# Kernel optimization log

Hardware: AMD Instinct MI355X
Metric: run time of the kernel (lower is better)

The kernel has to match this reference:

```python
import jax, jax.numpy as jnp
import numpy as np

NSTEPS = 20
ALPHA, BETA = 0.9, 0.85


def setup_inputs() -> dict:
    key = jax.random.key(0)
    ks = jax.random.split(key, 12)
    B, T, D_in, K, OUT = 64, NSTEPS, 16384, 25, 2
    dims = [8192, 4096, 2048]      # floor(dim/factor) per layer, factor=2
    prev = [16384, 8192, 4096]     # fan-in width each layer gathers from
    std = (2.0 / K) ** 0.5
    inp = {"x": jax.random.normal(ks[0], (B, T, D_in), jnp.float32)}
    for i, (d, p) in enumerate(zip(dims, prev)):
        inp[f"W{i}"] = jax.random.normal(ks[1 + i], (d, K), jnp.float32) * std
        inp[f"b{i}"] = jnp.zeros((1, d), jnp.float32)
        inp[f"knn{i}"] = jax.random.randint(ks[4 + i], (d, K), 0, p)
        inp[f"thr{i}"] = jax.random.uniform(ks[7 + i], (d,), jnp.float32)
    inp["Wfc"] = jax.random.normal(ks[10], (OUT, dims[-1]), jnp.float32) * dims[-1] ** -0.5
    inp["bfc"] = jnp.zeros((OUT,), jnp.float32)
    return inp


def reference(x, W0, b0, W1, b1, W2, b2, knn0, knn1, knn2,
              thr0, thr1, thr2, Wfc, bfc):
    # x: (B, T, D_in) -> scan over T
    Ws, bs = (W0, W1, W2), (b0, b1, b2)
    knns, thrs = (knn0, knn1, knn2), (thr0, thr1, thr2)
    n_layer = 3
    B = x.shape[0]
    xs = jnp.transpose(x, (1, 0, 2))  # (T, B, D_in)
    mems0 = tuple(jnp.zeros((B, w.shape[0]), x.dtype) for w in Ws)

    def step(mems, xt):
        h = xt
        new_mems, mem_recs, spk_recs = [], [], []
        for i in range(n_layer):
            g = h[:, knns[i]]                             # (B, dim_i, K) gather
            cur = jnp.einsum('bdk,dk->bd', g, Ws[i]) + bs[i]
            thr, mem_prev = thrs[i], mems[i]
            reset = (mem_prev > thr).astype(h.dtype)
            # NOTE: original code never writes the returned syn back, so the
            # synaptic state stays at zero init: syn = alpha*0 + cur = cur.
            syn = cur
            mem = BETA * mem_prev + syn - reset * thr
            spk = (mem - thr > 0).astype(h.dtype)
            if i == n_layer - 1:
                h = mem                 # last layer passes membrane forward
                new_mems.append(mem_prev)  # last-layer carry never updated
            else:
                h = spk
                new_mems.append(mem)
            mem_recs.append(mem)
            spk_recs.append(spk)
        angle = h @ Wfc.T + bfc
        return tuple(new_mems), (tuple(mem_recs), tuple(spk_recs), angle)

    _, (mem_rec, spk_rec, angles_all) = jax.lax.scan(step, mems0, xs)
    angles = angles_all[-1]  # original keeps only the last step's angle
    return (*mem_rec, *spk_rec, angles)
```

## Files before the change

kernel.cpp:

```cpp
#include <hip/hip_runtime.h>

#define NSTEPS 20
#define BATCH 64
#define D_IN 16384
#define KNN 25
#define BETA 0.85

#define D0 8192
#define D1 4096
#define D2 2048

#define NRT 24

__global__ void __launch_bounds__(256) transpose_x_kernel(
    const float* __restrict__ x, float* __restrict__ xT) {
  __shared__ float tile[64][65];
  const int t = blockIdx.y;
  const int d0 = blockIdx.x * 64;
  {
    const int dd4 = (threadIdx.x & 15) * 4;
    const int br = threadIdx.x >> 4;
#pragma unroll
    for (int i = 0; i < 4; ++i) {
      const int b = br + 16 * i;
      const float4 v = *reinterpret_cast<const float4*>(
          &x[((size_t)b * NSTEPS + t) * D_IN + d0 + dd4]);
      tile[b][dd4 + 0] = v.x;
      tile[b][dd4 + 1] = v.y;
      tile[b][dd4 + 2] = v.z;
      tile[b][dd4 + 3] = v.w;
    }
  }
  __syncthreads();
  {
    const int b = threadIdx.x & 63;
    const int dg = threadIdx.x >> 6;
#pragma unroll
    for (int i = 0; i < 16; ++i) {
      const int d = dg * 16 + i;
      xT[((size_t)t * D_IN + d0 + d) * BATCH + b] = tile[b][d];
    }
  }
}

template <bool IS_U8>
__global__ void __launch_bounds__(512) cur_kernel(
    const void* __restrict__ src, size_t st_t, const float* __restrict__ W,
    const float* __restrict__ bias, const int* __restrict__ knn, int dn,
    int dchunk0, double* __restrict__ curbuf) {
  const int nb_d = dn >> 4;
  const int g = blockIdx.x & 7;
  const int q = blockIdx.x >> 3;
  const int r = q / nb_d;
  const int i = q - r * nb_d;
  const int t = r * 8 + g;
  if (t >= NSTEPS) return;

  const int lane = threadIdx.x & 63;
  const int wv = threadIdx.x >> 6;
  const int dl0 = i * 16 + wv * 2;

#pragma unroll
  for (int j = 0; j < 2; ++j) {
    const int dl = dl0 + j;
    const int dg = __builtin_amdgcn_readfirstlane(dchunk0 + dl);
    const int* kp = knn + (size_t)dg * KNN;
    const float* wp = W + (size_t)dg * KNN;
    double cur = (double)bias[dg];
    if (IS_U8) {
      const unsigned char* sp =
          (const unsigned char*)src + (size_t)t * st_t + lane;
#pragma unroll
      for (int k = 0; k < KNN; ++k) {
        const int idx = kp[k];
        cur += (double)wp[k] * (double)sp[(size_t)idx * BATCH];
      }
    } else {
      const float* sp = (const float*)src + (size_t)t * st_t + lane;
#pragma unroll
      for (int k = 0; k < KNN; ++k) {
        const int idx = kp[k];
        cur += (double)wp[k] * (double)sp[(size_t)idx * BATCH];
      }
    }
    curbuf[((size_t)t * dn + dl) * BATCH + lane] = cur;
  }
}

__global__ void __launch_bounds__(512) scan_kernel(
    const double* __restrict__ curbuf, int dn, int dchunk0, int D,
    const float* __restrict__ thr, float* __restrict__ mem_rec,
    float* __restrict__ spk_rec, unsigned char* __restrict__ spkT) {
  __shared__ float s_mem[16][68];
  __shared__ float s_spk[16][68];
  const int dl0 = blockIdx.x * 16;
  const int lane = threadIdx.x & 63;
  const int wv = threadIdx.x >> 6;
  const int dbase = dl0 + wv * 2;

  double mem[2] = {0.0, 0.0};
  double thrv[2];
#pragma unroll
  for (int j = 0; j < 2; ++j) thrv[j] = (double)thr[dchunk0 + dbase + j];

  for (int t = 0; t < NSTEPS; ++t) {
#pragma unroll
    for (int j = 0; j < 2; ++j) {
      const int dl = dbase + j;
      const double cur = curbuf[((size_t)t * dn + dl) * BATCH + lane];
      double m = mem[j];
      const double reset = (m > thrv[j]) ? thrv[j] : 0.0;
      m = BETA * m + cur - reset;
      mem[j] = m;
      const float spk = (m > thrv[j]) ? 1.0f : 0.0f;
      s_mem[wv * 2 + j][lane] = (float)m;
      s_spk[wv * 2 + j][lane] = spk;
      if (spkT)
        spkT[((size_t)t * D + dchunk0 + dl) * BATCH + lane] =
            (unsigned char)spk;
    }
    __syncthreads();
    {
      const int dd = threadIdx.x & 15;
      const int bq = threadIdx.x >> 4;
#pragma unroll
      for (int i = 0; i < 2; ++i) {
        const int b = bq + 32 * i;
        const size_t o = ((size_t)t * BATCH + b) * D + dchunk0 + dl0 + dd;
        mem_rec[o] = s_mem[dd][b];
        spk_rec[o] = s_spk[dd][b];
      }
    }
    __syncthreads();
  }
}

template <bool IS_U8, bool CARRY>
__global__ void __launch_bounds__(512) layer_scan_kernel(
    const void* __restrict__ src, size_t st_t, size_t st_b, size_t st_idx,
    const float* __restrict__ W, const float* __restrict__ bias,
    const int* __restrict__ knn, const float* __restrict__ thr, int D,
    float* __restrict__ mem_rec, float* __restrict__ spk_rec,
    unsigned char* __restrict__ spkT) {
  __shared__ float s_mem[16][68];
  __shared__ float s_spk[16][68];
  const int d0 = blockIdx.x * 16;
  const int lane = threadIdx.x & 63;
  const int wv = threadIdx.x >> 6;
  const int dbase = d0 + wv * 2;

  double mem[2] = {0.0, 0.0};
  double thrv[2], bsv[2];
#pragma unroll
  for (int j = 0; j < 2; ++j) {
    thrv[j] = (double)thr[dbase + j];
    bsv[j] = (double)bias[dbase + j];
  }

  const int t_lo = CARRY ? 0 : (int)blockIdx.y;
  const int t_hi = CARRY ? NSTEPS : (int)blockIdx.y + 1;

  for (int t = t_lo; t < t_hi; ++t) {
#pragma unroll
    for (int j = 0; j < 2; ++j) {
      const int d = dbase + j;
      const int* kp = knn + (size_t)d * KNN;
      const float* wp = W + (size_t)d * KNN;
      const size_t base = (size_t)t * st_t + (size_t)lane * st_b;
      double cur = bsv[j];
#pragma unroll
      for (int k = 0; k < KNN; ++k) {
        const int idx = kp[k];
        if (IS_U8) {
          const unsigned char s =
              ((const unsigned char*)src)[base + (size_t)idx * st_idx];
          cur += (double)wp[k] * (double)s;
        } else {
          const float g = ((const float*)src)[base + (size_t)idx * st_idx];
          cur += (double)wp[k] * (double)g;
        }
      }
      double m = CARRY ? mem[j] : 0.0;
      const double reset = (m > thrv[j]) ? thrv[j] : 0.0;
      m = BETA * m + cur - reset;
      mem[j] = m;
      const float spk = (m > thrv[j]) ? 1.0f : 0.0f;
      s_mem[wv * 2 + j][lane] = (float)m;
      s_spk[wv * 2 + j][lane] = spk;
      if (spkT) spkT[((size_t)t * D + d) * BATCH + lane] = (unsigned char)spk;
    }
    __syncthreads();
    {
      const int dd = threadIdx.x & 15;
      const int bq = threadIdx.x >> 4;
#pragma unroll
      for (int i = 0; i < 2; ++i) {
        const int b = bq + 32 * i;
        const size_t o = ((size_t)t * BATCH + b) * D + d0 + dd;
        mem_rec[o] = s_mem[dd][b];
        spk_rec[o] = s_spk[dd][b];
      }
    }
    __syncthreads();
  }
}

__global__ void __launch_bounds__(64) fc_kernel(
    const float* __restrict__ mem2, const float* __restrict__ Wfc,
    const float* __restrict__ bfc, float* __restrict__ angles) {
  const int b = blockIdx.x;
  const float* h = mem2 + ((size_t)(NSTEPS - 1) * BATCH + b) * D2;
  double a0 = 0.0, a1 = 0.0;
  for (int d = threadIdx.x; d < D2; d += 64) {
    const double m = (double)h[d];
    a0 += m * (double)Wfc[d];
    a1 += m * (double)Wfc[D2 + d];
  }
#pragma unroll
  for (int off = 32; off > 0; off >>= 1) {
    a0 += __shfl_down(a0, off);
    a1 += __shfl_down(a1, off);
  }
  if (threadIdx.x == 0) {
    angles[(size_t)b * 2 + 0] = (float)(a0 + (double)bfc[0]);
    angles[(size_t)b * 2 + 1] = (float)(a1 + (double)bfc[1]);
  }
}

extern "C" void kernel_launch(void* const* d_in, const int* in_sizes, int n_in,
                              void* d_out, int out_size, void* d_ws,
                              size_t ws_size, hipStream_t stream) {
  const float* x = (const float*)d_in[0];
  const float* W0 = (const float*)d_in[1];
  const float* b0 = (const float*)d_in[2];
  const int* knn0 = (const int*)d_in[3];
  const float* thr0 = (const float*)d_in[4];
  const float* W1 = (const float*)d_in[5];
  const float* b1 = (const float*)d_in[6];
  const int* knn1 = (const int*)d_in[7];
  const float* thr1 = (const float*)d_in[8];
  const float* W2 = (const float*)d_in[9];
  const float* b2 = (const float*)d_in[10];
  const int* knn2 = (const int*)d_in[11];
  const float* thr2 = (const float*)d_in[12];
  const float* Wfc = (const float*)d_in[13];
  const float* bfc = (const float*)d_in[14];

  float* out = (float*)d_out;
  float* mem_rec0 = out;
  float* mem_rec1 = mem_rec0 + (size_t)NSTEPS * BATCH * D0;
  float* mem_rec2 = mem_rec1 + (size_t)NSTEPS * BATCH * D1;
  float* spk_rec0 = mem_rec2 + (size_t)NSTEPS * BATCH * D2;
  float* spk_rec1 = spk_rec0 + (size_t)NSTEPS * BATCH * D0;
  float* spk_rec2 = spk_rec1 + (size_t)NSTEPS * BATCH * D1;
  float* angles = spk_rec2 + (size_t)NSTEPS * BATCH * D2;

  const size_t xT_bytes = (size_t)NSTEPS * D_IN * BATCH * sizeof(float);
  const size_t s0_bytes = (size_t)NSTEPS * D0 * BATCH;
  const size_t s1_bytes = (size_t)NSTEPS * D1 * BATCH;
  const size_t base_bytes = xT_bytes + s0_bytes + s1_bytes;

  const bool planA = ws_size >= base_bytes;
  const bool planB = !planA && ws_size >= s0_bytes + s1_bytes;

  size_t leftover = (ws_size > base_bytes) ? ws_size - base_bytes : 0;
  int Dc = (int)((leftover / ((size_t)NSTEPS * BATCH * 8)) & ~(size_t)15);
  if (Dc > D0) Dc = D0;
  const bool planT = planA && Dc >= 512;

  const dim3 blk(512);

  if (planT) {
    float* xT = (float*)d_ws;
    unsigned char* spk0T = (unsigned char*)d_ws + xT_bytes;
    unsigned char* spk1T = spk0T + s0_bytes;
    double* curbuf = (double*)((char*)d_ws + base_bytes);

    transpose_x_kernel<<<dim3(D_IN / 64, NSTEPS), 256, 0, stream>>>(x, xT);

    for (int c0 = 0; c0 < D0; c0 += Dc) {
      const int dn = (D0 - c0 < Dc) ? (D0 - c0) : Dc;
      cur_kernel<false><<<dim3(NRT * (dn / 16)), blk, 0, stream>>>(
          xT, (size_t)D_IN * BATCH, W0, b0, knn0, dn, c0, curbuf);
      scan_kernel<<<dim3(dn / 16), blk, 0, stream>>>(
          curbuf, dn, c0, D0, thr0, mem_rec0, spk_rec0, spk0T);
    }
    for (int c0 = 0; c0 < D1; c0 += Dc) {
      const int dn = (D1 - c0 < Dc) ? (D1 - c0) : Dc;
      cur_kernel<true><<<dim3(NRT * (dn / 16)), blk, 0, stream>>>(
          spk0T, (size_t)D0 * BATCH, W1, b1, knn1, dn, c0, curbuf);
      scan_kernel<<<dim3(dn / 16), blk, 0, stream>>>(
          curbuf, dn, c0, D1, thr1, mem_rec1, spk_rec1, spk1T);
    }
    layer_scan_kernel<true, false><<<dim3(D2 / 16, NSTEPS), blk, 0, stream>>>(
        spk1T, (size_t)D1 * BATCH, 1, BATCH, W2, b2, knn2, thr2, D2, mem_rec2,
        spk_rec2, nullptr);
  } else if (planA) {
    float* xT = (float*)d_ws;
    unsigned char* spk0T = (unsigned char*)d_ws + xT_bytes;
    unsigned char* spk1T = spk0T + s0_bytes;

    transpose_x_kernel<<<dim3(D_IN / 64, NSTEPS), 256, 0, stream>>>(x, xT);
    layer_scan_kernel<false, true><<<dim3(D0 / 16), blk, 0, stream>>>(
        xT, (size_t)D_IN * BATCH, 1, BATCH, W0, b0, knn0, thr0, D0, mem_rec0,
        spk_rec0, spk0T);
    layer_scan_kernel<true, true><<<dim3(D1 / 16), blk, 0, stream>>>(
        spk0T, (size_t)D0 * BATCH, 1, BATCH, W1, b1, knn1, thr1, D1, mem_rec1,
        spk_rec1, spk1T);
    layer_scan_kernel<true, false><<<dim3(D2 / 16, NSTEPS), blk, 0, stream>>>(
        spk1T, (size_t)D1 * BATCH, 1, BATCH, W2, b2, knn2, thr2, D2, mem_rec2,
        spk_rec2, nullptr);
  } else if (planB) {
    unsigned char* spk0T = (unsigned char*)d_ws;
    unsigned char* spk1T = spk0T + s0_bytes;

    layer_scan_kernel<false, true><<<dim3(D0 / 16), blk, 0, stream>>>(
        x, (size_t)D_IN, (size_t)NSTEPS * D_IN, 1, W0, b0, knn0, thr0, D0,
        mem_rec0, spk_rec0, spk0T);
    layer_scan_kernel<true, true><<<dim3(D1 / 16), blk, 0, stream>>>(
        spk0T, (size_t)D0 * BATCH, 1, BATCH, W1, b1, knn1, thr1, D1, mem_rec1,
        spk_rec1, spk1T);
    layer_scan_kernel<true, false><<<dim3(D2 / 16, NSTEPS), blk, 0, stream>>>(
        spk1T, (size_t)D1 * BATCH, 1, BATCH, W2, b2, knn2, thr2, D2, mem_rec2,
        spk_rec2, nullptr);
  } else {
    layer_scan_kernel<false, true><<<dim3(D0 / 16), blk, 0, stream>>>(
        x, (size_t)D_IN, (size_t)NSTEPS * D_IN, 1, W0, b0, knn0, thr0, D0,
        mem_rec0, spk_rec0, nullptr);
    layer_scan_kernel<false, true><<<dim3(D1 / 16), blk, 0, stream>>>(
        spk_rec0, (size_t)BATCH * D0, (size_t)D0, 1, W1, b1, knn1, thr1, D1,
        mem_rec1, spk_rec1, nullptr);
    layer_scan_kernel<false, false><<<dim3(D2 / 16, NSTEPS), blk, 0, stream>>>(
        spk_rec1, (size_t)BATCH * D1, (size_t)D1, 1, W2, b2, knn2, thr2, D2,
        mem_rec2, spk_rec2, nullptr);
  }

  fc_kernel<<<dim3(BATCH), 64, 0, stream>>>(mem_rec2, Wfc, bfc, angles);
}
```

Before: 241.9 us.

## Fuse layer-1 gather-matvec and LIF scan into one kernel

Layer 1 previously ran as chunked pairs of a current kernel (spread over NRT blocks per chunk) followed by a scan kernel, with currents staged through a global double buffer. A new kernel now computes all 20 timesteps of current per neuron in registers from the u8 spike gather and runs the membrane recurrence in place. This removes the curbuf round trip and several launches. In exchange it uses only D1/16 = 256 blocks with a large per-thread register array, which lowers parallelism and occupancy.

```diff
diff --git a/kernel.cpp b/kernel.cpp
--- a/kernel.cpp
+++ b/kernel.cpp
@@ -127,6 +127,76 @@
       for (int i = 0; i < 2; ++i) {
         const int b = bq + 32 * i;
         const size_t o = ((size_t)t * BATCH + b) * D + dchunk0 + dl0 + dd;
+        mem_rec[o] = s_mem[dd][b];
+        spk_rec[o] = s_spk[dd][b];
+      }
+    }
+    __syncthreads();
+  }
+}
+
+__global__ void __launch_bounds__(512) lif_fused_u8_kernel(
+    const unsigned char* __restrict__ src, size_t st_t,
+    const float* __restrict__ W, const float* __restrict__ bias,
+    const int* __restrict__ knn, const float* __restrict__ thr, int D,
+    float* __restrict__ mem_rec, float* __restrict__ spk_rec,
+    unsigned char* __restrict__ spkT) {
+  __shared__ float s_mem[16][68];
+  __shared__ float s_spk[16][68];
+  const int d0 = blockIdx.x * 16;
+  const int lane = threadIdx.x & 63;
+  const int wv = threadIdx.x >> 6;
+  const int dbase = d0 + wv * 2;
+
+  double cur[2][NSTEPS];
+  double thrv[2];
+#pragma unroll
+  for (int j = 0; j < 2; ++j) {
+    const int d = __builtin_amdgcn_readfirstlane(dbase + j);
+    thrv[j] = (double)thr[d];
+    const double bs = (double)bias[d];
+#pragma unroll
+    for (int t = 0; t < NSTEPS; ++t) cur[j][t] = bs;
+  }
+
+#pragma unroll
+  for (int j = 0; j < 2; ++j) {
+    const int d = __builtin_amdgcn_readfirstlane(dbase + j);
+    const int* kp = knn + (size_t)d * KNN;
+    const float* wp = W + (size_t)d * KNN;
+#pragma unroll 5
+    for (int k = 0; k < KNN; ++k) {
+      const int idx = kp[k];
+      const double w = (double)wp[k];
+      const unsigned char* sp = src + (size_t)idx * BATCH + lane;
+#pragma unroll
+      for (int t = 0; t < NSTEPS; ++t)
+        cur[j][t] += w * (double)sp[(size_t)t * st_t];
+    }
+  }
+
+  double mem[2] = {0.0, 0.0};
+#pragma unroll
+  for (int t = 0; t < NSTEPS; ++t) {
+#pragma unroll
+    for (int j = 0; j < 2; ++j) {
+      double m = mem[j];
+      const double reset = (m > thrv[j]) ? thrv[j] : 0.0;
+      m = BETA * m + cur[j][t] - reset;
+      mem[j] = m;
+      const float spk = (m > thrv[j]) ? 1.0f : 0.0f;
+      s_mem[wv * 2 + j][lane] = (float)m;
+      s_spk[wv * 2 + j][lane] = spk;
+      spkT[((size_t)t * D + dbase + j) * BATCH + lane] = (unsigned char)spk;
+    }
+    __syncthreads();
+    {
+      const int dd = threadIdx.x & 15;
+      const int bq = threadIdx.x >> 4;
+#pragma unroll
+      for (int i = 0; i < 2; ++i) {
+        const int b = bq + 32 * i;
+        const size_t o = ((size_t)t * BATCH + b) * D + d0 + dd;
         mem_rec[o] = s_mem[dd][b];
         spk_rec[o] = s_spk[dd][b];
       }
@@ -285,13 +355,9 @@
       scan_kernel<<<dim3(dn / 16), blk, 0, stream>>>(
           curbuf, dn, c0, D0, thr0, mem_rec0, spk_rec0, spk0T);
     }
-    for (int c0 = 0; c0 < D1; c0 += Dc) {
-      const int dn = (D1 - c0 < Dc) ? (D1 - c0) : Dc;
-      cur_kernel<true><<<dim3(NRT * (dn / 16)), blk, 0, stream>>>(
-          spk0T, (size_t)D0 * BATCH, W1, b1, knn1, dn, c0, curbuf);
-      scan_kernel<<<dim3(dn / 16), blk, 0, stream>>>(
-          curbuf, dn, c0, D1, thr1, mem_rec1, spk_rec1, spk1T);
-    }
+    lif_fused_u8_kernel<<<dim3(D1 / 16), blk, 0, stream>>>(
+        spk0T, (size_t)D0 * BATCH, W1, b1, knn1, thr1, D1, mem_rec1,
+        spk_rec1, spk1T);
     layer_scan_kernel<true, false><<<dim3(D2 / 16, NSTEPS), blk, 0, stream>>>(
         spk1T, (size_t)D1 * BATCH, 1, BATCH, W2, b2, knn2, thr2, D2, mem_rec2,
         spk_rec2, nullptr);
```

After: 460.4 us. 1.9x slower.
